# Optimization experiments

Measured on AMD Instinct MI355X. Metric: run time of the kernel, lower is better.

Reference implementation:

```python
import jax, jax.numpy as jnp
import numpy as np

B, T, C = 4, 2048, 2048
N, K = 16, 4          # query heads, kv heads
G, H = N // K, C // N # group size 4, head dim 128


def _rmsnorm(x):
    # RMSNorm over the full last (flattened N*H or K*H) axis, no scale param
    var = jnp.mean(jnp.square(x.astype(jnp.float32)), axis=-1, keepdims=True)
    return (x * jax.lax.rsqrt(var + 1e-06)).astype(x.dtype)


def _sine_table(features, length, max_timescale=10000.0):
    fraction = jnp.arange(0, features, 2, dtype=jnp.float32) / features
    timescale = max_timescale ** fraction
    sinusoid = jnp.einsum('i,j->ij', jnp.arange(length).astype(jnp.float32), 1.0 / timescale,
                          precision=jax.lax.Precision.HIGHEST)
    sinusoid = jnp.concatenate([sinusoid, sinusoid], axis=-1)  # [T, H]
    return jnp.sin(sinusoid), jnp.cos(sinusoid)


def _rotate_half(x):
    x1, x2 = jnp.split(x, 2, axis=-1)
    return jnp.concatenate([-x2, x1], axis=-1)


def setup_inputs() -> dict:
    key = jax.random.key(0)
    kx, kq, kk, kv, ko = jax.random.split(key, 5)
    q_std = float(np.sqrt(2.0 / (5.0 * C)))
    o_std = 2.0 / 24 / float(np.sqrt(N * H))  # wang init, n_layers=24
    return {
        'x': jax.random.normal(kx, (B, T, C), dtype=jnp.float32),
        'Wq': jax.random.normal(kq, (C, N * H), dtype=jnp.float32) * q_std,
        'Wk': jax.random.normal(kk, (C, K * H), dtype=jnp.float32) * q_std,
        'Wv': jax.random.normal(kv, (C, K * H), dtype=jnp.float32) * q_std,
        'Wout': jax.random.normal(ko, (N * H, C), dtype=jnp.float32) * o_std,
    }


def reference(x, Wq, Wk, Wv, Wout):
    b, t, c = x.shape
    q = _rmsnorm(x @ Wq)              # [B,T,N*H]
    k = _rmsnorm(x @ Wk)              # [B,T,K*H]
    v = x @ Wv                        # [B,T,K*H]
    q = q.reshape(b, t, K, G, H)
    k = k.reshape(b, t, K, H)
    v = v.reshape(b, t, K, H)

    sin, cos = _sine_table(H, t)      # [T,H]
    qcos, qsin = cos[None, :, None, None, :], sin[None, :, None, None, :]
    kcos, ksin = cos[None, :, None, :], sin[None, :, None, :]
    q = (q * qcos + _rotate_half(q) * qsin).astype(q.dtype)
    k = (k * kcos + _rotate_half(k) * ksin).astype(k.dtype)

    scale = jax.lax.rsqrt(jnp.array(H, dtype=jnp.float32)).astype(q.dtype)
    q = q * scale
    # full (non-causal) softmax attention; GQA: each kv head serves G query groups
    logits = jnp.einsum('btkgh,bskh->bkgts', q, k)
    probs = jax.nn.softmax(logits.astype(jnp.float32), axis=-1).astype(logits.dtype)
    enc = jnp.einsum('bkgts,bskh->btkgh', probs, v)  # [B,T,K,G,H]
    return enc.reshape(b, t, N * H) @ Wout
```

## Files before the change

kernel.cpp:

```cpp
#include <hip/hip_runtime.h>
#include <hip/hip_bf16.h>
#include <math.h>

typedef __attribute__((ext_vector_type(4))) float f32x4;
typedef __attribute__((ext_vector_type(8))) short s16x8;
typedef __attribute__((ext_vector_type(4))) short s16x4;

#define BB 4
#define TT 2048
#define CC 2048
#define NHEAD 16
#define KVH 4
#define HD 128
#define BT (BB*TT)
#define NHC 2048
#define KHC 512
#define QKVC 3072

__device__ __forceinline__ float bf2f(unsigned short u) {
  union { unsigned u; float f; } v; v.u = ((unsigned)u) << 16; return v.f;
}
__device__ __forceinline__ unsigned short f2bf(float f) {
  union { float f; unsigned u; } v; v.f = f;
  unsigned r = v.u + 0x7fff + ((v.u >> 16) & 1);
  return (unsigned short)(r >> 16);
}

#if defined(__has_builtin)
#if __has_builtin(__builtin_amdgcn_exp2f)
#define EXP2F(x) __builtin_amdgcn_exp2f(x)
#endif
#endif
#ifndef EXP2F
#define EXP2F(x) exp2f(x)
#endif

__device__ __forceinline__ void glld16(const void* gsrc, void* ldsbase) {
  __builtin_amdgcn_global_load_lds(
      (const __attribute__((address_space(1))) unsigned int*)gsrc,
      (__attribute__((address_space(3))) unsigned int*)(unsigned int)(unsigned long long)ldsbase,
      16, 0, 0);
}

__global__ void cvt_f2b(const float* __restrict__ in, unsigned short* __restrict__ out, int n4) {
  int i = blockIdx.x * 256 + threadIdx.x;
  if (i >= n4) return;
  float4 v = ((const float4*)in)[i];
  ushort4 o;
  o.x = f2bf(v.x); o.y = f2bf(v.y); o.z = f2bf(v.z); o.w = f2bf(v.w);
  ((ushort4*)out)[i] = o;
}

__global__ void trans_f2b(const float* __restrict__ in, unsigned short* __restrict__ out, int R, int Cc) {
  __shared__ float tile[32][33];
  int c0 = blockIdx.x * 32, r0 = blockIdx.y * 32;
  int tx = threadIdx.x, ty = threadIdx.y;
  #pragma unroll
  for (int k = 0; k < 4; k++)
    tile[ty + 8*k][tx] = in[(size_t)(r0 + ty + 8*k) * Cc + c0 + tx];
  __syncthreads();
  #pragma unroll
  for (int k = 0; k < 4; k++)
    out[(size_t)(c0 + ty + 8*k) * R + r0 + tx] = f2bf(tile[tx][ty + 8*k]);
}

__global__ void trans_v(const unsigned short* __restrict__ qkv, unsigned short* __restrict__ vT) {
  __shared__ unsigned short tile[32][33];
  int slice = blockIdx.z;
  int s0 = blockIdx.x * 32, h0 = blockIdx.y * 32;
  int tx = threadIdx.x, ty = threadIdx.y;
  const unsigned short* in = qkv + (size_t)(slice >> 2) * TT * QKVC + (NHC + KHC) + (slice & 3) * HD;
  unsigned short* out = vT + (size_t)slice * HD * TT;
  #pragma unroll
  for (int k = 0; k < 4; k++)
    tile[ty + 8*k][tx] = in[(size_t)(s0 + ty + 8*k) * QKVC + h0 + tx];
  __syncthreads();
  #pragma unroll
  for (int k = 0; k < 4; k++)
    out[(size_t)(h0 + ty + 8*k) * TT + s0 + tx] = tile[tx][ty + 8*k];
}

__global__ void sincos_init(float* __restrict__ stab, float* __restrict__ ctab) {
  int idx = blockIdx.x * 256 + threadIdx.x;
  if (idx >= TT * 64) return;
  int t = idx >> 6, i = idx & 63;
  double inv = exp(-log(10000.0) * ((double)i / 64.0));
  double ang = (double)t * inv;
  stab[idx] = (float)sin(ang);
  ctab[idx] = (float)cos(ang);
}

template<int OUTBF16>
__global__ __launch_bounds__(512, 2) void gemm256(
    const unsigned short* __restrict__ A, const unsigned short* __restrict__ Bt,
    void* __restrict__ outp, int M, int Nn, int Kd) {
  __shared__ unsigned short As[2][256 * 64];
  __shared__ unsigned short Bs[2][256 * 64];
  int tid = threadIdx.x;
  int wave = tid >> 6, lane = tid & 63, q4 = lane >> 4, l16 = lane & 15;

  int gx = Nn >> 8;
  int nwg = gridDim.x;
  int bid = blockIdx.x;
  int bid2 = (nwg & 7) ? bid : ((bid & 7) * (nwg >> 3) + (bid >> 3));
  int bx = bid2 % gx, by = bid2 / gx;
  int m0 = by * 256, n0 = bx * 256;

  int wm = (wave >> 2) * 128;
  int wn = (wave & 3) * 64;

  f32x4 acc[8][4];
  #pragma unroll
  for (int i = 0; i < 8; i++)
    #pragma unroll
    for (int j = 0; j < 4; j++) acc[i][j] = f32x4{0.f, 0.f, 0.f, 0.f};

  const unsigned short* Abase = A + (size_t)m0 * Kd;
  const unsigned short* Bbase = Bt + (size_t)n0 * Kd;

  auto stage = [&](const unsigned short* Ak, const unsigned short* Bk, int buf) {
    #pragma unroll
    for (int t = 0; t < 4; t++) {
      int cf = (wave * 4 + t) * 64 + lane;
      int r = cf >> 3, cg = (cf & 7) ^ (r & 7);
      glld16(Ak + (size_t)r * Kd + cg * 8, &As[buf][(wave * 4 + t) * 512]);
    }
    #pragma unroll
    for (int t = 0; t < 4; t++) {
      int cf = (wave * 4 + t) * 64 + lane;
      int r = cf >> 3, cg = (cf & 7) ^ (r & 7);
      glld16(Bk + (size_t)r * Kd + cg * 8, &Bs[buf][(wave * 4 + t) * 512]);
    }
  };

  stage(Abase, Bbase, 0);
  __syncthreads();

  int nkt = Kd >> 6;
  for (int kt = 0; kt < nkt; kt++) {
    int cur = kt & 1;
    if (kt + 1 < nkt) stage(Abase + (kt + 1) * 64, Bbase + (kt + 1) * 64, cur ^ 1);
    #pragma unroll
    for (int ks = 0; ks < 2; ks++) {
      s16x8 af[8], bfv[4];
      int c = ks * 4 + q4;
      #pragma unroll
      for (int mf = 0; mf < 8; mf++) {
        int r = wm + mf * 16 + l16;
        af[mf] = *(const s16x8*)&As[cur][r * 64 + ((c ^ (r & 7)) << 3)];
      }
      #pragma unroll
      for (int nf = 0; nf < 4; nf++) {
        int r = wn + nf * 16 + l16;
        bfv[nf] = *(const s16x8*)&Bs[cur][r * 64 + ((c ^ (r & 7)) << 3)];
      }
      __builtin_amdgcn_s_setprio(1);
      #pragma unroll
      for (int mf = 0; mf < 8; mf++)
        #pragma unroll
        for (int nf = 0; nf < 4; nf++)
          acc[mf][nf] = __builtin_amdgcn_mfma_f32_16x16x32_bf16(af[mf], bfv[nf], acc[mf][nf], 0, 0, 0);
      __builtin_amdgcn_s_setprio(0);
    }
    __syncthreads();
  }

  #pragma unroll
  for (int mf = 0; mf < 8; mf++)
    #pragma unroll
    for (int nf = 0; nf < 4; nf++)
      #pragma unroll
      for (int r = 0; r < 4; r++) {
        int row = m0 + wm + mf * 16 + q4 * 4 + r;
        int col = n0 + wn + nf * 16 + l16;
        float v = acc[mf][nf][r];
        if (OUTBF16) ((unsigned short*)outp)[(size_t)row * Nn + col] = f2bf(v);
        else         ((float*)outp)[(size_t)row * Nn + col] = v;
      }
}

__global__ __launch_bounds__(256) void postproc(
    const unsigned short* __restrict__ qkv, unsigned short* __restrict__ qr,
    unsigned short* __restrict__ kr, const float* __restrict__ stab, const float* __restrict__ ctab) {
  __shared__ float sh[NHC + KHC];
  __shared__ float redq[4], redk[4];
  int row = blockIdx.x;
  int t = row & (TT - 1);
  int tid = threadIdx.x;
  const unsigned short* base = qkv + (size_t)row * QKVC;
  float sq = 0.f, sk = 0.f;
  uint4 qv = *(const uint4*)&base[tid * 8];
  const unsigned short* qp = (const unsigned short*)&qv;
  #pragma unroll
  for (int i = 0; i < 8; i++) { float f = bf2f(qp[i]); sh[tid*8 + i] = f; sq += f*f; }
  unsigned kv = *(const unsigned*)&base[NHC + tid*2];
  {
    float f0 = bf2f((unsigned short)(kv & 0xffff));
    float f1 = bf2f((unsigned short)(kv >> 16));
    sh[NHC + tid*2] = f0; sh[NHC + tid*2 + 1] = f1;
    sk += f0*f0 + f1*f1;
  }
  #pragma unroll
  for (int off = 32; off > 0; off >>= 1) { sq += __shfl_xor(sq, off); sk += __shfl_xor(sk, off); }
  if ((tid & 63) == 0) { redq[tid >> 6] = sq; redk[tid >> 6] = sk; }
  __syncthreads();
  float fq = rsqrtf((redq[0]+redq[1]+redq[2]+redq[3]) * (1.f/NHC) + 1e-6f)
             * (0.08838834764831845f * 1.4426950408889634f);
  float fk = rsqrtf((redk[0]+redk[1]+redk[2]+redk[3]) * (1.f/KHC) + 1e-6f);
  #pragma unroll
  for (int pi = 0; pi < 4; pi++) {
    int P = pi * 256 + tid;
    int head = P >> 6, i = P & 63;
    float s = stab[t*64 + i], c = ctab[t*64 + i];
    float x1 = sh[head*128 + i], x2 = sh[head*128 + i + 64];
    qr[(size_t)row * NHC + head*128 + i]      = f2bf((x1*c - x2*s) * fq);
    qr[(size_t)row * NHC + head*128 + i + 64] = f2bf((x2*c + x1*s) * fq);
  }
  {
    int head = tid >> 6, i = tid & 63;
    float s = stab[t*64 + i], c = ctab[t*64 + i];
    float x1 = sh[NHC + head*128 + i], x2 = sh[NHC + head*128 + i + 64];
    kr[(size_t)row * KHC + head*128 + i]      = f2bf((x1*c - x2*s) * fk);
    kr[(size_t)row * KHC + head*128 + i + 64] = f2bf((x2*c + x1*s) * fk);
  }
}

__global__ __launch_bounds__(256, 2) void attn(
    const unsigned short* __restrict__ qr, const unsigned short* __restrict__ kr,
    const unsigned short* __restrict__ vT, unsigned short* __restrict__ enc) {
  __shared__ unsigned short Ks[2][64 * 128];
  __shared__ unsigned short Vs[2][128 * 64];
  int tid = threadIdx.x;
  int wave = tid >> 6, lane = tid & 63, q4 = lane >> 4, l16 = lane & 15;
  int bid = blockIdx.x;
  int qt = bid & 15, n = (bid >> 4) & 15, b = bid >> 8, kh = n >> 2;

  const unsigned short* kbase = kr + ((size_t)(b * TT)) * KHC + kh * HD;
  const unsigned short* vbase = vT + ((size_t)((b * KVH + kh) * HD)) * TT;

  auto stageK = [&](int j, int kb) {
    const unsigned short* base = kbase + (size_t)(j * 64) * KHC;
    #pragma unroll
    for (int t = 0; t < 4; t++) {
      int L = wave * 4 + t;
      int r = L * 4 + (lane >> 4);
      int cg = (lane & 15) ^ (r & 7);
      glld16(base + (size_t)r * KHC + cg * 8, &Ks[kb][L * 512]);
    }
  };
  auto stageV = [&](int j, int vb) {
    const unsigned short* base = vbase + j * 64;
    #pragma unroll
    for (int t = 0; t < 4; t++) {
      int L = wave * 4 + t;
      int r = L * 8 + (lane >> 3);
      int cg = (lane & 7) ^ (r & 7);
      glld16(base + (size_t)r * TT + cg * 8, &Vs[vb][L * 512]);
    }
  };

  {
    const unsigned short* base = qr + ((size_t)(b * TT + qt * 128)) * NHC + n * HD;
    #pragma unroll
    for (int t = 0; t < 8; t++) {
      int L = wave * 8 + t;
      int r = L * 4 + (lane >> 4);
      int cg = (lane & 15) ^ (r & 7);
      glld16(base + (size_t)r * NHC + cg * 8, (unsigned short*)Ks + L * 512);
    }
  }
  stageV(0, 0);
  asm volatile("s_waitcnt vmcnt(0)" ::: "memory");
  __syncthreads();
  s16x8 qf[2][4];
  #pragma unroll
  for (int qb = 0; qb < 2; qb++)
    #pragma unroll
    for (int ku = 0; ku < 4; ku++) {
      int r = wave * 32 + qb * 16 + l16;
      qf[qb][ku] = *(const s16x8*)&((const unsigned short*)Ks)[r * 128 + (((ku * 4 + q4) ^ (r & 7)) << 3)];
    }
  __syncthreads();
  stageK(0, 0);
  asm volatile("s_waitcnt vmcnt(0)" ::: "memory");
  __syncthreads();

  float m_st[2] = {-1e30f, -1e30f}, l_st[2] = {0.f, 0.f};
  f32x4 O[2][8];
  #pragma unroll
  for (int qb = 0; qb < 2; qb++)
    #pragma unroll
    for (int hb = 0; hb < 8; hb++) O[qb][hb] = f32x4{0.f, 0.f, 0.f, 0.f};

  for (int j = 0; j < 32; j++) {
    int cur = j & 1;
    if (j < 31) { stageK(j + 1, cur ^ 1); stageV(j + 1, cur ^ 1); }
    f32x4 S[2][4];
    #pragma unroll
    for (int qb = 0; qb < 2; qb++)
      #pragma unroll
      for (int mb = 0; mb < 4; mb++) S[qb][mb] = f32x4{0.f, 0.f, 0.f, 0.f};
    __builtin_amdgcn_s_setprio(1);
    #pragma unroll
    for (int mb = 0; mb < 4; mb++) {
      int r = mb * 16 + l16;
      #pragma unroll
      for (int ku = 0; ku < 4; ku++) {
        s16x8 kf = *(const s16x8*)&Ks[cur][r * 128 + (((ku * 4 + q4) ^ (r & 7)) << 3)];
        S[0][mb] = __builtin_amdgcn_mfma_f32_16x16x32_bf16(kf, qf[0][ku], S[0][mb], 0, 0, 0);
        S[1][mb] = __builtin_amdgcn_mfma_f32_16x16x32_bf16(kf, qf[1][ku], S[1][mb], 0, 0, 0);
      }
    }
    __builtin_amdgcn_s_setprio(0);
    s16x8 pf8[2][2];
    #pragma unroll
    for (int qb = 0; qb < 2; qb++) {
      float mx = -1e30f;
      #pragma unroll
      for (int mb = 0; mb < 4; mb++)
        #pragma unroll
        for (int r = 0; r < 4; r++) mx = fmaxf(mx, S[qb][mb][r]);
      mx = fmaxf(mx, __shfl_xor(mx, 16));
      mx = fmaxf(mx, __shfl_xor(mx, 32));
      if (!__all(mx - m_st[qb] <= 8.f)) {
        float alpha = EXP2F(m_st[qb] - mx);
        m_st[qb] = mx;
        l_st[qb] *= alpha;
        #pragma unroll
        for (int hb = 0; hb < 8; hb++) O[qb][hb] *= alpha;
      }
      float mcur = m_st[qb];
      float rs = 0.f;
      #pragma unroll
      for (int mb = 0; mb < 4; mb++)
        #pragma unroll
        for (int r = 0; r < 4; r++) {
          float p = EXP2F(S[qb][mb][r] - mcur);
          rs += p;
          pf8[qb][mb >> 1][(mb & 1) * 4 + r] = (short)f2bf(p);
        }
      rs += __shfl_xor(rs, 16);
      rs += __shfl_xor(rs, 32);
      l_st[qb] += rs;
    }
    __builtin_amdgcn_s_setprio(1);
    #pragma unroll
    for (int su = 0; su < 2; su++) {
      #pragma unroll
      for (int hb = 0; hb < 8; hb++) {
        int r = hb * 16 + l16;
        int c0 = su * 8 + q4;
        int c1 = c0 + 4;
        s16x4 v0 = *(const s16x4*)&Vs[cur][r * 64 + (((c0 >> 1) ^ (r & 7)) << 3) + ((c0 & 1) << 2)];
        s16x4 v1 = *(const s16x4*)&Vs[cur][r * 64 + (((c1 >> 1) ^ (r & 7)) << 3) + ((c1 & 1) << 2)];
        s16x8 vf = __builtin_shufflevector(v0, v1, 0, 1, 2, 3, 4, 5, 6, 7);
        O[0][hb] = __builtin_amdgcn_mfma_f32_16x16x32_bf16(vf, pf8[0][su], O[0][hb], 0, 0, 0);
        O[1][hb] = __builtin_amdgcn_mfma_f32_16x16x32_bf16(vf, pf8[1][su], O[1][hb], 0, 0, 0);
      }
    }
    __builtin_amdgcn_s_setprio(0);
    asm volatile("s_waitcnt vmcnt(0)" ::: "memory");
    __syncthreads();
  }
  #pragma unroll
  for (int qb = 0; qb < 2; qb++) {
    float inv = 1.f / l_st[qb];
    int t = b * TT + qt * 128 + wave * 32 + qb * 16 + l16;
    #pragma unroll
    for (int hb = 0; hb < 8; hb++) {
      ushort4 o;
      o.x = f2bf(O[qb][hb][0] * inv);
      o.y = f2bf(O[qb][hb][1] * inv);
      o.z = f2bf(O[qb][hb][2] * inv);
      o.w = f2bf(O[qb][hb][3] * inv);
      *(ushort4*)&enc[(size_t)t * NHC + n * HD + hb * 16 + q4 * 4] = o;
    }
  }
}

extern "C" void kernel_launch(void* const* d_in, const int* in_sizes, int n_in,
                              void* d_out, int out_size, void* d_ws, size_t ws_size,
                              hipStream_t stream) {
  const float* x  = (const float*)d_in[0];
  const float* Wq = (const float*)d_in[1];
  const float* Wk = (const float*)d_in[2];
  const float* Wv = (const float*)d_in[3];
  const float* Wo = (const float*)d_in[4];
  float* out = (float*)d_out;

  char* ws = (char*)d_ws;
  size_t off = 0;
  auto alloc = [&](size_t bytes) -> void* {
    void* p = ws + off;
    off += (bytes + 255) & ~(size_t)255;
    return p;
  };
  unsigned short* xb    = (unsigned short*)alloc((size_t)BT * CC * 2);
  unsigned short* wqkvt = (unsigned short*)alloc((size_t)QKVC * CC * 2);
  unsigned short* wot   = (unsigned short*)alloc((size_t)CC * NHC * 2);
  unsigned short* qkv   = (unsigned short*)alloc((size_t)BT * QKVC * 2);
  unsigned short* qrb   = (unsigned short*)alloc((size_t)BT * NHC * 2);
  unsigned short* krb   = (unsigned short*)alloc((size_t)BT * KHC * 2);
  unsigned short* vTb   = (unsigned short*)alloc((size_t)BB * KVH * HD * TT * 2);
  unsigned short* encb  = (unsigned short*)alloc((size_t)BT * NHC * 2);
  float* stab = (float*)alloc((size_t)TT * 64 * 4);
  float* ctab = (float*)alloc((size_t)TT * 64 * 4);

  dim3 tb(32, 8);
  cvt_f2b<<<(BT*CC/4 + 255)/256, 256, 0, stream>>>(x, xb, BT*CC/4);
  trans_f2b<<<dim3(NHC/32, CC/32), tb, 0, stream>>>(Wq, wqkvt, CC, NHC);
  trans_f2b<<<dim3(KHC/32, CC/32), tb, 0, stream>>>(Wk, wqkvt + (size_t)NHC*CC, CC, KHC);
  trans_f2b<<<dim3(KHC/32, CC/32), tb, 0, stream>>>(Wv, wqkvt + (size_t)(NHC+KHC)*CC, CC, KHC);
  trans_f2b<<<dim3(NHC/32, NHC/32), tb, 0, stream>>>(Wo, wot, NHC, CC);
  sincos_init<<<(TT*64 + 255)/256, 256, 0, stream>>>(stab, ctab);
  gemm256<1><<<(BT/256) * (QKVC/256), 512, 0, stream>>>(xb, wqkvt, qkv, BT, QKVC, CC);
  postproc<<<BT, 256, 0, stream>>>(qkv, qrb, krb, stab, ctab);
  trans_v<<<dim3(TT/32, HD/32, BB*KVH), tb, 0, stream>>>(qkv, vTb);
  attn<<<BB * NHEAD * (TT/128), 256, 0, stream>>>(qrb, krb, vTb, encb);
  gemm256<0><<<(BT/256) * (CC/256), 512, 0, stream>>>(encb, wot, out, BT, CC, NHC);
}
```

Baseline: 525.4 us.

## Deepen GEMM pipeline to four K=32 LDS stages with vmcnt-based waits

Reworks the 256x256 GEMM mainloop from a double-buffered K=64 tile into a four-buffer ring of K=32 tiles, with three tiles in flight. A partial s_waitcnt vmcnt plus a raw s_barrier replaces the full __syncthreads, so global loads overlap more MFMA work. The swizzled LDS offsets and per-thread load addresses are precomputed once outside the loop. The risks are more barriers per unit of K, and correctness now depends on the hand-counted vmcnt values matching the compiler's actual load count.

```diff
diff --git a/kernel.cpp b/kernel.cpp
--- a/kernel.cpp
+++ b/kernel.cpp
@@ -94,8 +94,8 @@
 __global__ __launch_bounds__(512, 2) void gemm256(
     const unsigned short* __restrict__ A, const unsigned short* __restrict__ Bt,
     void* __restrict__ outp, int M, int Nn, int Kd) {
-  __shared__ unsigned short As[2][256 * 64];
-  __shared__ unsigned short Bs[2][256 * 64];
+  __shared__ unsigned short As[4][256 * 32];
+  __shared__ unsigned short Bs[4][256 * 32];
   int tid = threadIdx.x;
   int wave = tid >> 6, lane = tid & 63, q4 = lane >> 4, l16 = lane & 15;
 
@@ -118,51 +118,66 @@
   const unsigned short* Abase = A + (size_t)m0 * Kd;
   const unsigned short* Bbase = Bt + (size_t)n0 * Kd;
 
-  auto stage = [&](const unsigned short* Ak, const unsigned short* Bk, int buf) {
-    #pragma unroll
-    for (int t = 0; t < 4; t++) {
-      int cf = (wave * 4 + t) * 64 + lane;
-      int r = cf >> 3, cg = (cf & 7) ^ (r & 7);
-      glld16(Ak + (size_t)r * Kd + cg * 8, &As[buf][(wave * 4 + t) * 512]);
-    }
-    #pragma unroll
-    for (int t = 0; t < 4; t++) {
-      int cf = (wave * 4 + t) * 64 + lane;
-      int r = cf >> 3, cg = (cf & 7) ^ (r & 7);
-      glld16(Bk + (size_t)r * Kd + cg * 8, &Bs[buf][(wave * 4 + t) * 512]);
-    }
+  int sR[2], sCG[2], sBase[2];
+  #pragma unroll
+  for (int rd = 0; rd < 2; rd++) {
+    int L = rd * 512 + wave * 64 + lane;
+    int srow = L >> 3, eff = L & 7;
+    int slot8 = eff ^ (srow & 7);
+    sR[rd] = srow * 2 + (slot8 >> 2);
+    sCG[rd] = slot8 & 3;
+    sBase[rd] = (rd * 512 + wave * 64) * 8;
+  }
+  auto stage = [&](int kt, int buf) {
+    const unsigned short* Ak = Abase + kt * 32;
+    const unsigned short* Bk = Bbase + kt * 32;
+    #pragma unroll
+    for (int rd = 0; rd < 2; rd++)
+      glld16(Ak + (size_t)sR[rd] * Kd + sCG[rd] * 8, &As[buf][sBase[rd]]);
+    #pragma unroll
+    for (int rd = 0; rd < 2; rd++)
+      glld16(Bk + (size_t)sR[rd] * Kd + sCG[rd] * 8, &Bs[buf][sBase[rd]]);
   };
 
-  stage(Abase, Bbase, 0);
-  __syncthreads();
-
-  int nkt = Kd >> 6;
-  for (int kt = 0; kt < nkt; kt++) {
-    int cur = kt & 1;
-    if (kt + 1 < nkt) stage(Abase + (kt + 1) * 64, Bbase + (kt + 1) * 64, cur ^ 1);
-    #pragma unroll
-    for (int ks = 0; ks < 2; ks++) {
-      s16x8 af[8], bfv[4];
-      int c = ks * 4 + q4;
-      #pragma unroll
-      for (int mf = 0; mf < 8; mf++) {
-        int r = wm + mf * 16 + l16;
-        af[mf] = *(const s16x8*)&As[cur][r * 64 + ((c ^ (r & 7)) << 3)];
-      }
-      #pragma unroll
-      for (int nf = 0; nf < 4; nf++) {
-        int r = wn + nf * 16 + l16;
-        bfv[nf] = *(const s16x8*)&Bs[cur][r * 64 + ((c ^ (r & 7)) << 3)];
-      }
-      __builtin_amdgcn_s_setprio(1);
-      #pragma unroll
-      for (int mf = 0; mf < 8; mf++)
-        #pragma unroll
-        for (int nf = 0; nf < 4; nf++)
-          acc[mf][nf] = __builtin_amdgcn_mfma_f32_16x16x32_bf16(af[mf], bfv[nf], acc[mf][nf], 0, 0, 0);
-      __builtin_amdgcn_s_setprio(0);
-    }
-    __syncthreads();
+  int aoffs[8], boffs[4];
+  #pragma unroll
+  for (int mf = 0; mf < 8; mf++) {
+    int R = wm + mf * 16 + l16;
+    int srow = R >> 1;
+    aoffs[mf] = (srow * 8 + ((((R & 1) << 2) | q4) ^ (srow & 7))) * 8;
+  }
+  #pragma unroll
+  for (int nf = 0; nf < 4; nf++) {
+    int R = wn + nf * 16 + l16;
+    int srow = R >> 1;
+    boffs[nf] = (srow * 8 + ((((R & 1) << 2) | q4) ^ (srow & 7))) * 8;
+  }
+
+  int nkt = Kd >> 5;
+  stage(0, 0);
+  stage(1, 1);
+  stage(2, 2);
+
+  for (int t = 0; t < nkt; t++) {
+    int cur = t & 3;
+    if (t < nkt - 2)       asm volatile("s_waitcnt vmcnt(8)" ::: "memory");
+    else if (t == nkt - 2) asm volatile("s_waitcnt vmcnt(4)" ::: "memory");
+    else                   asm volatile("s_waitcnt vmcnt(0)" ::: "memory");
+    asm volatile("s_barrier" ::: "memory");
+    if (t + 3 < nkt) stage(t + 3, (t + 3) & 3);
+
+    s16x8 af[8], bfv[4];
+    #pragma unroll
+    for (int mf = 0; mf < 8; mf++) af[mf] = *(const s16x8*)&As[cur][aoffs[mf]];
+    #pragma unroll
+    for (int nf = 0; nf < 4; nf++) bfv[nf] = *(const s16x8*)&Bs[cur][boffs[nf]];
+    __builtin_amdgcn_s_setprio(1);
+    #pragma unroll
+    for (int mf = 0; mf < 8; mf++)
+      #pragma unroll
+      for (int nf = 0; nf < 4; nf++)
+        acc[mf][nf] = __builtin_amdgcn_mfma_f32_16x16x32_bf16(af[mf], bfv[nf], acc[mf][nf], 0, 0, 0);
+    __builtin_amdgcn_s_setprio(0);
   }
 
   #pragma unroll
```

New measurement: 521.6 us. About the same (-0.7%).

## Hand-schedule GEMM main loop with split staging and barrier-phased MFMA

Applied to the files above, without the earlier changes.

Rewrites the bf16 GEMM inner loop into four barrier-separated phases per K tile. Each phase issues explicit ds_read_b128 fragment loads, interleaves half-tile global-to-LDS copies (B for the next tile, A two tiles ahead), and then runs a block of MFMAs at raised priority. Source pointers are precomputed, and vmcnt waits are tuned so loads stay in flight across iterations. The aim is to overlap LDS reads, global prefetch and MFMA work more tightly than the compiler-scheduled version. In exchange it adds many more s_barrier points and relies on fragile hand-counted waitcnt logic.

```diff
diff --git a/kernel.cpp b/kernel.cpp
--- a/kernel.cpp
+++ b/kernel.cpp
@@ -42,6 +42,14 @@
       16, 0, 0);
 }
 
+__device__ __forceinline__ s16x8 lds_read_b128(unsigned addr) {
+  s16x8 r;
+  asm volatile("ds_read_b128 %0, %1" : "=v"(r) : "v"(addr));
+  return r;
+}
+
+#define MFMA_BF16(a, b, c) __builtin_amdgcn_mfma_f32_16x16x32_bf16((a), (b), (c), 0, 0, 0)
+
 __global__ void cvt_f2b(const float* __restrict__ in, unsigned short* __restrict__ out, int n4) {
   int i = blockIdx.x * 256 + threadIdx.x;
   if (i >= n4) return;
@@ -105,9 +113,7 @@
   int bid2 = (nwg & 7) ? bid : ((bid & 7) * (nwg >> 3) + (bid >> 3));
   int bx = bid2 % gx, by = bid2 / gx;
   int m0 = by * 256, n0 = bx * 256;
-
-  int wm = (wave >> 2) * 128;
-  int wn = (wave & 3) * 64;
+  int wm = (wave >> 2) * 128, wn = (wave & 3) * 64;
 
   f32x4 acc[8][4];
   #pragma unroll
@@ -115,54 +121,111 @@
     #pragma unroll
     for (int j = 0; j < 4; j++) acc[i][j] = f32x4{0.f, 0.f, 0.f, 0.f};
 
-  const unsigned short* Abase = A + (size_t)m0 * Kd;
-  const unsigned short* Bbase = Bt + (size_t)n0 * Kd;
-
-  auto stage = [&](const unsigned short* Ak, const unsigned short* Bk, int buf) {
-    #pragma unroll
-    for (int t = 0; t < 4; t++) {
-      int cf = (wave * 4 + t) * 64 + lane;
-      int r = cf >> 3, cg = (cf & 7) ^ (r & 7);
-      glld16(Ak + (size_t)r * Kd + cg * 8, &As[buf][(wave * 4 + t) * 512]);
-    }
-    #pragma unroll
-    for (int t = 0; t < 4; t++) {
-      int cf = (wave * 4 + t) * 64 + lane;
-      int r = cf >> 3, cg = (cf & 7) ^ (r & 7);
-      glld16(Bk + (size_t)r * Kd + cg * 8, &Bs[buf][(wave * 4 + t) * 512]);
-    }
+  const unsigned short* Asrc[2][2];
+  const unsigned short* Bsrc[2][2];
+  #pragma unroll
+  for (int h = 0; h < 2; h++)
+    #pragma unroll
+    for (int ld = 0; ld < 2; ld++) {
+      int L = h * 1024 + wave * 128 + ld * 64 + lane;
+      int r = L >> 3, cg = (L & 7) ^ (r & 7);
+      Asrc[h][ld] = A + (size_t)(m0 + r) * Kd + cg * 8;
+      Bsrc[h][ld] = Bt + (size_t)(n0 + r) * Kd + cg * 8;
+    }
+  auto stageA = [&](int kt, int h) {
+    unsigned short* d = &As[kt & 1][(h * 1024 + wave * 128) * 8];
+    glld16(Asrc[h][0] + (size_t)kt * 64, d);
+    glld16(Asrc[h][1] + (size_t)kt * 64, d + 512);
   };
-
-  stage(Abase, Bbase, 0);
-  __syncthreads();
+  auto stageB = [&](int kt, int h) {
+    unsigned short* d = &Bs[kt & 1][(h * 1024 + wave * 128) * 8];
+    glld16(Bsrc[h][0] + (size_t)kt * 64, d);
+    glld16(Bsrc[h][1] + (size_t)kt * 64, d + 512);
+  };
+
+  unsigned asB = (unsigned)(unsigned long long)(void*)&As[0][0];
+  unsigned bsB = (unsigned)(unsigned long long)(void*)&Bs[0][0];
+  int aRow = (wm + l16) * 128;
+  int bRow = (wn + l16) * 128;
+  int slot0 = ((0 + q4) ^ (l16 & 7)) * 16;
+  int slot1 = ((4 + q4) ^ (l16 & 7)) * 16;
 
   int nkt = Kd >> 6;
+  stageA(0, 0); stageA(0, 1); stageB(0, 0); stageB(0, 1);
+  stageA(1, 0); stageA(1, 1);
+  asm volatile("s_waitcnt vmcnt(4)" ::: "memory");
+  asm volatile("s_barrier" ::: "memory");
+
   for (int kt = 0; kt < nkt; kt++) {
-    int cur = kt & 1;
-    if (kt + 1 < nkt) stage(Abase + (kt + 1) * 64, Bbase + (kt + 1) * 64, cur ^ 1);
-    #pragma unroll
-    for (int ks = 0; ks < 2; ks++) {
-      s16x8 af[8], bfv[4];
-      int c = ks * 4 + q4;
-      #pragma unroll
-      for (int mf = 0; mf < 8; mf++) {
-        int r = wm + mf * 16 + l16;
-        af[mf] = *(const s16x8*)&As[cur][r * 64 + ((c ^ (r & 7)) << 3)];
-      }
-      #pragma unroll
-      for (int nf = 0; nf < 4; nf++) {
-        int r = wn + nf * 16 + l16;
-        bfv[nf] = *(const s16x8*)&Bs[cur][r * 64 + ((c ^ (r & 7)) << 3)];
-      }
-      __builtin_amdgcn_s_setprio(1);
-      #pragma unroll
-      for (int mf = 0; mf < 8; mf++)
-        #pragma unroll
-        for (int nf = 0; nf < 4; nf++)
-          acc[mf][nf] = __builtin_amdgcn_mfma_f32_16x16x32_bf16(af[mf], bfv[nf], acc[mf][nf], 0, 0, 0);
-      __builtin_amdgcn_s_setprio(0);
-    }
-    __syncthreads();
+    unsigned aT = asB + (kt & 1) * 32768 + aRow;
+    unsigned bT = bsB + (kt & 1) * 32768 + bRow;
+    s16x8 af0[8], af1[8], bf0, bf1;
+
+    #pragma unroll
+    for (int mf = 0; mf < 8; mf++) af0[mf] = lds_read_b128(aT + slot0 + mf * 2048);
+    bf0 = lds_read_b128(bT + slot0);
+    bf1 = lds_read_b128(bT + slot0 + 2048);
+    if (kt + 1 < nkt) stageB(kt + 1, 0);
+    asm volatile("s_barrier" ::: "memory");
+    asm volatile("s_waitcnt lgkmcnt(0)" ::: "memory");
+    __builtin_amdgcn_sched_barrier(0);
+    __builtin_amdgcn_s_setprio(1);
+    #pragma unroll
+    for (int mf = 0; mf < 8; mf++) {
+      acc[mf][0] = MFMA_BF16(af0[mf], bf0, acc[mf][0]);
+      acc[mf][1] = MFMA_BF16(af0[mf], bf1, acc[mf][1]);
+    }
+    __builtin_amdgcn_s_setprio(0);
+    asm volatile("s_barrier" ::: "memory");
+
+    #pragma unroll
+    for (int mf = 0; mf < 8; mf++) af1[mf] = lds_read_b128(aT + slot1 + mf * 2048);
+    bf0 = lds_read_b128(bT + slot0 + 2 * 2048);
+    bf1 = lds_read_b128(bT + slot0 + 3 * 2048);
+    if (kt + 1 < nkt) stageB(kt + 1, 1);
+    asm volatile("s_barrier" ::: "memory");
+    asm volatile("s_waitcnt lgkmcnt(0)" ::: "memory");
+    __builtin_amdgcn_sched_barrier(0);
+    __builtin_amdgcn_s_setprio(1);
+    #pragma unroll
+    for (int mf = 0; mf < 8; mf++) {
+      acc[mf][2] = MFMA_BF16(af0[mf], bf0, acc[mf][2]);
+      acc[mf][3] = MFMA_BF16(af0[mf], bf1, acc[mf][3]);
+    }
+    __builtin_amdgcn_s_setprio(0);
+    asm volatile("s_barrier" ::: "memory");
+
+    bf0 = lds_read_b128(bT + slot1);
+    bf1 = lds_read_b128(bT + slot1 + 2048);
+    if (kt + 2 < nkt) stageA(kt + 2, 0);
+    asm volatile("s_barrier" ::: "memory");
+    asm volatile("s_waitcnt lgkmcnt(0)" ::: "memory");
+    __builtin_amdgcn_sched_barrier(0);
+    __builtin_amdgcn_s_setprio(1);
+    #pragma unroll
+    for (int mf = 0; mf < 8; mf++) {
+      acc[mf][0] = MFMA_BF16(af1[mf], bf0, acc[mf][0]);
+      acc[mf][1] = MFMA_BF16(af1[mf], bf1, acc[mf][1]);
+    }
+    __builtin_amdgcn_s_setprio(0);
+    asm volatile("s_barrier" ::: "memory");
+
+    bf0 = lds_read_b128(bT + slot1 + 2 * 2048);
+    bf1 = lds_read_b128(bT + slot1 + 3 * 2048);
+    if (kt + 2 < nkt) stageA(kt + 2, 1);
+    if (kt < nkt - 2) asm volatile("s_waitcnt vmcnt(4)" ::: "memory");
+    else              asm volatile("s_waitcnt vmcnt(0)" ::: "memory");
+    asm volatile("s_barrier" ::: "memory");
+    asm volatile("s_waitcnt lgkmcnt(0)" ::: "memory");
+    __builtin_amdgcn_sched_barrier(0);
+    __builtin_amdgcn_s_setprio(1);
+    #pragma unroll
+    for (int mf = 0; mf < 8; mf++) {
+      acc[mf][2] = MFMA_BF16(af1[mf], bf0, acc[mf][2]);
+      acc[mf][3] = MFMA_BF16(af1[mf], bf1, acc[mf][3]);
+    }
+    __builtin_amdgcn_s_setprio(0);
+    asm volatile("s_barrier" ::: "memory");
   }
 
   #pragma unroll
```

After: 530.2 us. Within noise of the previous version (+0.9%).

## Use 32x32x16 MFMA in GEMM and packed bf16 conversion in attention

Applied to the files above, without the earlier changes.

The GEMM inner loop switches from 16x16x32 to 32x32x16 bf16 MFMA tiles, so each wave issues fewer, larger matrix instructions and performs fewer LDS fragment reads per k-step; the epilogue row and column mapping is updated to match the 32x32 accumulator layout. The attention kernel replaces the software round-to-nearest f32-to-bf16 conversion with the hardware v_cvt_pk_bf16_f32 instruction for the probability fragments and the output stores. This reduces ALU work in the softmax path. The hardware conversion may handle rounding or NaNs slightly differently from the software routine.

```diff
diff --git a/kernel.cpp b/kernel.cpp
--- a/kernel.cpp
+++ b/kernel.cpp
@@ -3,6 +3,7 @@
 #include <math.h>
 
 typedef __attribute__((ext_vector_type(4))) float f32x4;
+typedef __attribute__((ext_vector_type(16))) float f32x16;
 typedef __attribute__((ext_vector_type(8))) short s16x8;
 typedef __attribute__((ext_vector_type(4))) short s16x4;
 
@@ -25,6 +26,11 @@
   unsigned r = v.u + 0x7fff + ((v.u >> 16) & 1);
   return (unsigned short)(r >> 16);
 }
+__device__ __forceinline__ unsigned cvt_pk_bf16(float lo, float hi) {
+  unsigned r;
+  asm("v_cvt_pk_bf16_f32 %0, %1, %2" : "=v"(r) : "v"(lo), "v"(hi));
+  return r;
+}
 
 #if defined(__has_builtin)
 #if __has_builtin(__builtin_amdgcn_exp2f)
@@ -97,7 +103,8 @@
   __shared__ unsigned short As[2][256 * 64];
   __shared__ unsigned short Bs[2][256 * 64];
   int tid = threadIdx.x;
-  int wave = tid >> 6, lane = tid & 63, q4 = lane >> 4, l16 = lane & 15;
+  int wave = tid >> 6, lane = tid & 63;
+  int l32 = lane & 31, khf = lane >> 5;
 
   int gx = Nn >> 8;
   int nwg = gridDim.x;
@@ -105,15 +112,15 @@
   int bid2 = (nwg & 7) ? bid : ((bid & 7) * (nwg >> 3) + (bid >> 3));
   int bx = bid2 % gx, by = bid2 / gx;
   int m0 = by * 256, n0 = bx * 256;
-
-  int wm = (wave >> 2) * 128;
-  int wn = (wave & 3) * 64;
-
-  f32x4 acc[8][4];
-  #pragma unroll
-  for (int i = 0; i < 8; i++)
-    #pragma unroll
-    for (int j = 0; j < 4; j++) acc[i][j] = f32x4{0.f, 0.f, 0.f, 0.f};
+  int wm = (wave >> 2) * 128, wn = (wave & 3) * 64;
+
+  f32x16 acc[4][2];
+  #pragma unroll
+  for (int i = 0; i < 4; i++)
+    #pragma unroll
+    for (int j = 0; j < 2; j++)
+      #pragma unroll
+      for (int r = 0; r < 16; r++) acc[i][j][r] = 0.f;
 
   const unsigned short* Abase = A + (size_t)m0 * Kd;
   const unsigned short* Bbase = Bt + (size_t)n0 * Kd;
@@ -141,38 +148,38 @@
     int cur = kt & 1;
     if (kt + 1 < nkt) stage(Abase + (kt + 1) * 64, Bbase + (kt + 1) * 64, cur ^ 1);
     #pragma unroll
-    for (int ks = 0; ks < 2; ks++) {
-      s16x8 af[8], bfv[4];
-      int c = ks * 4 + q4;
-      #pragma unroll
-      for (int mf = 0; mf < 8; mf++) {
-        int r = wm + mf * 16 + l16;
-        af[mf] = *(const s16x8*)&As[cur][r * 64 + ((c ^ (r & 7)) << 3)];
-      }
-      #pragma unroll
-      for (int nf = 0; nf < 4; nf++) {
-        int r = wn + nf * 16 + l16;
-        bfv[nf] = *(const s16x8*)&Bs[cur][r * 64 + ((c ^ (r & 7)) << 3)];
+    for (int ks = 0; ks < 4; ks++) {
+      int c = ks * 2 + khf;
+      s16x8 af[4], bfv[2];
+      #pragma unroll
+      for (int mf = 0; mf < 4; mf++) {
+        int R = wm + mf * 32 + l32;
+        af[mf] = *(const s16x8*)&As[cur][R * 64 + ((c ^ (R & 7)) << 3)];
+      }
+      #pragma unroll
+      for (int nf = 0; nf < 2; nf++) {
+        int R = wn + nf * 32 + l32;
+        bfv[nf] = *(const s16x8*)&Bs[cur][R * 64 + ((c ^ (R & 7)) << 3)];
       }
       __builtin_amdgcn_s_setprio(1);
       #pragma unroll
-      for (int mf = 0; mf < 8; mf++)
+      for (int mf = 0; mf < 4; mf++)
         #pragma unroll
-        for (int nf = 0; nf < 4; nf++)
-          acc[mf][nf] = __builtin_amdgcn_mfma_f32_16x16x32_bf16(af[mf], bfv[nf], acc[mf][nf], 0, 0, 0);
+        for (int nf = 0; nf < 2; nf++)
+          acc[mf][nf] = __builtin_amdgcn_mfma_f32_32x32x16_bf16(af[mf], bfv[nf], acc[mf][nf], 0, 0, 0);
       __builtin_amdgcn_s_setprio(0);
     }
     __syncthreads();
   }
 
   #pragma unroll
-  for (int mf = 0; mf < 8; mf++)
-    #pragma unroll
-    for (int nf = 0; nf < 4; nf++)
-      #pragma unroll
-      for (int r = 0; r < 4; r++) {
-        int row = m0 + wm + mf * 16 + q4 * 4 + r;
-        int col = n0 + wn + nf * 16 + l16;
+  for (int mf = 0; mf < 4; mf++)
+    #pragma unroll
+    for (int nf = 0; nf < 2; nf++)
+      #pragma unroll
+      for (int r = 0; r < 16; r++) {
+        int row = m0 + wm + mf * 32 + (r & 3) + 8 * (r >> 2) + 4 * khf;
+        int col = n0 + wn + nf * 32 + l32;
         float v = acc[mf][nf][r];
         if (OUTBF16) ((unsigned short*)outp)[(size_t)row * Nn + col] = f2bf(v);
         else         ((float*)outp)[(size_t)row * Nn + col] = v;
@@ -332,13 +339,21 @@
       float mcur = m_st[qb];
       float rs = 0.f;
       #pragma unroll
-      for (int mb = 0; mb < 4; mb++)
+      for (int su = 0; su < 2; su++) {
+        union { s16x8 v; unsigned d[4]; } pu;
         #pragma unroll
-        for (int r = 0; r < 4; r++) {
-          float p = EXP2F(S[qb][mb][r] - mcur);
-          rs += p;
-          pf8[qb][mb >> 1][(mb & 1) * 4 + r] = (short)f2bf(p);
+        for (int hf = 0; hf < 2; hf++) {
+          int mb = su * 2 + hf;
+          float p0 = EXP2F(S[qb][mb][0] - mcur);
+          float p1 = EXP2F(S[qb][mb][1] - mcur);
+          float p2 = EXP2F(S[qb][mb][2] - mcur);
+          float p3 = EXP2F(S[qb][mb][3] - mcur);
+          rs += (p0 + p1) + (p2 + p3);
+          pu.d[hf * 2 + 0] = cvt_pk_bf16(p0, p1);
+          pu.d[hf * 2 + 1] = cvt_pk_bf16(p2, p3);
         }
+        pf8[qb][su] = pu.v;
+      }
       rs += __shfl_xor(rs, 16);
       rs += __shfl_xor(rs, 32);
       l_st[qb] += rs;
@@ -368,12 +383,10 @@
     int t = b * TT + qt * 128 + wave * 32 + qb * 16 + l16;
     #pragma unroll
     for (int hb = 0; hb < 8; hb++) {
-      ushort4 o;
-      o.x = f2bf(O[qb][hb][0] * inv);
-      o.y = f2bf(O[qb][hb][1] * inv);
-      o.z = f2bf(O[qb][hb][2] * inv);
-      o.w = f2bf(O[qb][hb][3] * inv);
-      *(ushort4*)&enc[(size_t)t * NHC + n * HD + hb * 16 + q4 * 4] = o;
+      union { ushort4 s; unsigned d[2]; } o;
+      o.d[0] = cvt_pk_bf16(O[qb][hb][0] * inv, O[qb][hb][1] * inv);
+      o.d[1] = cvt_pk_bf16(O[qb][hb][2] * inv, O[qb][hb][3] * inv);
+      *(ushort4*)&enc[(size_t)t * NHC + n * HD + hb * 16 + q4 * 4] = o.s;
     }
   }
 }
```

New measurement: 520.7 us. About the same (-0.9%).
